# Kernel tuning notes

Hardware: AMD Instinct MI355X
Metric: run time of the kernel (lower is better)

Reference implementation:

```python
import jax, jax.numpy as jnp
import numpy as np

B, T, D, K = 4, 4096, 384, 64

def setup_inputs() -> dict:
    key = jax.random.key(0)
    k1, k2, k3, k4 = jax.random.split(key, 4)
    x = jax.random.normal(k1, (B, T, D), dtype=jnp.float32)
    # nn.Linear weights stored as (out_features, in_features); y = x @ W.T
    Wk = jax.random.normal(k2, (K, D), dtype=jnp.float32) * (1.0 / np.sqrt(D))
    Wq = jax.random.normal(k3, (K, D), dtype=jnp.float32) * (1.0 / np.sqrt(D))
    Wv = jax.random.normal(k4, (D, D), dtype=jnp.float32) * (1.0 / np.sqrt(D))
    return {"x": x, "Wk": Wk, "Wq": Wq, "Wv": Wv}

def reference(x, Wk, Wq, Wv):
    # x: (B,T,D)
    k = jnp.einsum('btd,kd->btk', x, Wk)   # (B,T,K)
    q = jnp.einsum('btd,kd->btk', x, Wq)   # (B,T,K)
    v = jnp.einsum('btd,ed->bte', x, Wv)   # (B,T,D)
    scores = jnp.einsum('btk,bsk->bts', q, k)  # (B,T,T)
    Tq = x.shape[1]
    causal = jnp.tril(jnp.ones((Tq, Tq), dtype=bool))[None, :, :]
    scores = jnp.where(causal, scores, -jnp.inf)
    w = jax.nn.softmax(scores / jnp.sqrt(jnp.asarray(Wk.shape[0], scores.dtype)), axis=-1)
    return jnp.einsum('bts,bsd->btd', w, v)  # (B,T,D)
```

## Files before the change

### kernel.cpp

```cpp
#include <hip/hip_runtime.h>


#define BB 4
#define TT 4096
#define DD 384

#define OWKA 0
#define OWQA 24576
#define OWVB 49152
#define OYK  196608
#define OYQ  1245184
#define OVT  2293760

#define C_EXP 0.18033688011112042f

typedef __bf16 bf16x8 __attribute__((ext_vector_type(8)));
typedef float f32x16 __attribute__((ext_vector_type(16)));
typedef unsigned short u16x4 __attribute__((ext_vector_type(4)));

__device__ __forceinline__ unsigned short f2bf(float f) {
  unsigned int u = __builtin_bit_cast(unsigned int, f);
  u += 0x7FFFu + ((u >> 16) & 1u);
  return (unsigned short)(u >> 16);
}

__device__ __forceinline__ bf16x8 ldb8(const unsigned short* p) {
  return *reinterpret_cast<const bf16x8*>(p);
}

__global__ __launch_bounds__(256) void convert_w(
    const float* __restrict__ Wk, const float* __restrict__ Wq,
    const float* __restrict__ Wv, unsigned short* __restrict__ ws) {
  int g = blockIdx.x * 256 + threadIdx.x;
  int row = g / 96;
  int fin = (g - row * 96) * 4;
  const float* src;
  unsigned short* dstbase;
  int m;
  if (row < 64)       { src = Wk + row * 384;         dstbase = ws + OWKA; m = row; }
  else if (row < 128) { src = Wq + (row - 64) * 384;  dstbase = ws + OWQA; m = row - 64; }
  else                { src = Wv + (row - 128) * 384; dstbase = ws + OWVB; m = row - 128; }
  float4 f = *reinterpret_cast<const float4*>(src + fin);
  u16x4 o;
  o[0] = f2bf(f.x); o[1] = f2bf(f.y); o[2] = f2bf(f.z); o[3] = f2bf(f.w);
  unsigned short* dst = dstbase + (m >> 5) * 12288 + (fin >> 4) * 512
                        + ((((fin >> 3) & 1) << 5) + (m & 31)) * 8 + (fin & 7);
  *reinterpret_cast<u16x4*>(dst) = o;
}

__global__ __launch_bounds__(512) void proj_fused(
    const float* __restrict__ x, const unsigned short* __restrict__ ws_r,
    unsigned short* __restrict__ Yk, unsigned short* __restrict__ Yq,
    unsigned short* __restrict__ Vt) {
  __shared__ __align__(16) unsigned short xlds[24576];
  int tb = blockIdx.x;
  int b = tb >> 6;
  int tid = threadIdx.x;
  {
    int r = tid >> 3, e = tid & 7;
    const float* xr = x + (tb * 64 + r) * DD + e * 48;
#pragma unroll
    for (int i = 0; i < 12; i++) {
      int fin = e * 48 + i * 4;
      float4 f = *reinterpret_cast<const float4*>(xr + i * 4);
      u16x4 o;
      o[0] = f2bf(f.x); o[1] = f2bf(f.y); o[2] = f2bf(f.z); o[3] = f2bf(f.w);
      unsigned short* dst = xlds + (r >> 5) * 12288 + (fin >> 4) * 512
                            + ((((fin >> 3) & 1) << 5) + (r & 31)) * 8 + (fin & 7);
      *reinterpret_cast<u16x4*>(dst) = o;
    }
  }
  __syncthreads();
  int wid = tid >> 6, lane = tid & 63;
  int l31 = lane & 31, h8 = lane >> 5;
  const f32x16 fz16 = {};
  if (wid < 2) {
    const unsigned short* Wa = ws_r + (wid ? OWQA : OWKA) + lane * 8;
    unsigned short* Ysel = (wid ? Yq : Yk);
    f32x16 acc[2][2];
    acc[0][0] = fz16; acc[0][1] = fz16; acc[1][0] = fz16; acc[1][1] = fz16;
    for (int ks = 0; ks < 24; ks++) {
      bf16x8 a0 = ldb8(Wa + ks * 512);
      bf16x8 a1 = ldb8(Wa + 12288 + ks * 512);
      bf16x8 b0 = ldb8(xlds + ks * 512 + lane * 8);
      bf16x8 b1 = ldb8(xlds + 12288 + ks * 512 + lane * 8);
      acc[0][0] = __builtin_amdgcn_mfma_f32_32x32x16_bf16(a0, b0, acc[0][0], 0, 0, 0);
      acc[0][1] = __builtin_amdgcn_mfma_f32_32x32x16_bf16(a0, b1, acc[0][1], 0, 0, 0);
      acc[1][0] = __builtin_amdgcn_mfma_f32_32x32x16_bf16(a1, b0, acc[1][0], 0, 0, 0);
      acc[1][1] = __builtin_amdgcn_mfma_f32_32x32x16_bf16(a1, b1, acc[1][1], 0, 0, 0);
    }
#pragma unroll
    for (int mt = 0; mt < 2; mt++)
#pragma unroll
      for (int nt = 0; nt < 2; nt++) {
        int tile = b * 128 + (tb & 63) * 2 + nt;
#pragma unroll
        for (int rg = 0; rg < 4; rg++) {
          u16x4 o;
#pragma unroll
          for (int i = 0; i < 4; i++) o[i] = f2bf(acc[mt][nt][rg * 4 + i]);
          *reinterpret_cast<u16x4*>(Ysel + tile * 2048 + (mt * 2 + (rg >> 1)) * 512
                                    + (((rg & 1) << 5) + l31) * 8 + 4 * h8) = o;
        }
      }
  } else {
    int vw = wid - 2;
    const unsigned short* Wb = ws_r + OWVB + vw * 2 * 12288 + lane * 8;
    f32x16 acc[2][2];
    acc[0][0] = fz16; acc[0][1] = fz16; acc[1][0] = fz16; acc[1][1] = fz16;
    for (int ks = 0; ks < 24; ks++) {
      bf16x8 a0 = ldb8(xlds + ks * 512 + lane * 8);
      bf16x8 a1 = ldb8(xlds + 12288 + ks * 512 + lane * 8);
      bf16x8 w0 = ldb8(Wb + ks * 512);
      bf16x8 w1 = ldb8(Wb + 12288 + ks * 512);
      acc[0][0] = __builtin_amdgcn_mfma_f32_32x32x16_bf16(a0, w0, acc[0][0], 0, 0, 0);
      acc[0][1] = __builtin_amdgcn_mfma_f32_32x32x16_bf16(a0, w1, acc[0][1], 0, 0, 0);
      acc[1][0] = __builtin_amdgcn_mfma_f32_32x32x16_bf16(a1, w0, acc[1][0], 0, 0, 0);
      acc[1][1] = __builtin_amdgcn_mfma_f32_32x32x16_bf16(a1, w1, acc[1][1], 0, 0, 0);
    }
    int k128 = (tb & 63) >> 1;
#pragma unroll
    for (int t32 = 0; t32 < 2; t32++)
#pragma unroll
      for (int dt = 0; dt < 2; dt++) {
        int dti = vw * 2 + dt;
        unsigned short* vbase = Vt + ((b * 12 + dti) * 32 + k128) * 4096;
#pragma unroll
        for (int rg = 0; rg < 4; rg++) {
          u16x4 o;
#pragma unroll
          for (int i = 0; i < 4; i++) o[i] = f2bf(acc[t32][dt][rg * 4 + i]);
          int kseg = 4 * (tb & 1) + t32 * 2 + (rg >> 1);
          *reinterpret_cast<u16x4*>(vbase + kseg * 512
                                    + (((rg & 1) << 5) + l31) * 8 + 4 * h8) = o;
        }
      }
  }
}

__global__ __launch_bounds__(256, 2) void flash_attn(
    const unsigned short* __restrict__ Yk, const unsigned short* __restrict__ Yq,
    const unsigned short* __restrict__ Vt, float* __restrict__ out) {
  __shared__ __align__(16) unsigned short pbuf[2][8192];
  __shared__ float lred[4][32];
  int blk = blockIdx.x;
  int xcd = blk & 7;
  int b = xcd >> 1, half = xcd & 1;
  int n = blk >> 3;
  int st = (n < 32) ? (127 - 2 * n - half) : (2 * (n - 32) + half);
  int wid = threadIdx.x >> 6, lane = threadIdx.x & 63;
  int l31 = lane & 31, h8 = lane >> 5;
  const f32x16 fz16 = {};
  const unsigned short* qbase = Yq + (b * 128 + st) * 2048 + lane * 8;
  bf16x8 qf[4];
#pragma unroll
  for (int ks = 0; ks < 4; ks++) qf[ks] = ldb8(qbase + ks * 512);
  f32x16 acc[3];
  acc[0] = fz16; acc[1] = fz16; acc[2] = fz16;
  float psum = 0.f;
  int n128 = (st >> 2) + 1;
  int qrow = st * 32 + l31;
  const unsigned short* kbase = Yk + (b * 128 + wid) * 2048 + lane * 8;
  const unsigned short* vbase = Vt + ((b * 12 + wid * 3) * 32) * 4096 + lane * 8;
#pragma unroll 1
  for (int kb = 0; kb < n128; kb++) {
    const unsigned short* kt = kbase + kb * 8192;
    bf16x8 kf[4];
#pragma unroll
    for (int ks = 0; ks < 4; ks++) kf[ks] = ldb8(kt + ks * 512);
    f32x16 sacc = fz16;
#pragma unroll
    for (int ks = 0; ks < 4; ks++)
      sacc = __builtin_amdgcn_mfma_f32_32x32x16_bf16(kf[ks], qf[ks], sacc, 0, 0, 0);
    int kg0 = kb * 128 + wid * 32 + 4 * h8;
    unsigned short* pw = pbuf[kb & 1];
#pragma unroll
    for (int rg = 0; rg < 4; rg++) {
      u16x4 o;
#pragma unroll
      for (int i = 0; i < 4; i++) {
        int key = kg0 + rg * 8 + i;
        float pv = (key > qrow) ? 0.f : exp2f(sacc[rg * 4 + i] * C_EXP);
        psum += pv;
        o[i] = f2bf(pv);
      }
      int g = wid * 2 + (rg >> 1);
      *reinterpret_cast<u16x4*>(pw + g * 512 + ((rg & 1) * 32 + l31) * 8 + 4 * h8) = o;
    }
    const unsigned short* vt = vbase + kb * 4096;
    bf16x8 vf0[8], vf1[8], vf2[8];
#pragma unroll
    for (int g = 0; g < 8; g++) vf0[g] = ldb8(vt + g * 512);
#pragma unroll
    for (int g = 0; g < 8; g++) vf1[g] = ldb8(vt + 32 * 4096 + g * 512);
#pragma unroll
    for (int g = 0; g < 8; g++) vf2[g] = ldb8(vt + 64 * 4096 + g * 512);
    __syncthreads();
    bf16x8 pf[8];
#pragma unroll
    for (int g = 0; g < 8; g++) pf[g] = ldb8(pw + g * 512 + lane * 8);
#pragma unroll
    for (int g = 0; g < 8; g++) {
      acc[0] = __builtin_amdgcn_mfma_f32_32x32x16_bf16(vf0[g], pf[g], acc[0], 0, 0, 0);
      acc[1] = __builtin_amdgcn_mfma_f32_32x32x16_bf16(vf1[g], pf[g], acc[1], 0, 0, 0);
      acc[2] = __builtin_amdgcn_mfma_f32_32x32x16_bf16(vf2[g], pf[g], acc[2], 0, 0, 0);
    }
  }
  psum += __shfl_xor(psum, 32);
  if (h8 == 0) lred[wid][l31] = psum;
  __syncthreads();
  float lt = lred[0][l31] + lred[1][l31] + lred[2][l31] + lred[3][l31];
  float inv = 1.0f / lt;
  float* ob = out + (b * TT + st * 32 + l31) * DD + wid * 96;
#pragma unroll
  for (int dt = 0; dt < 3; dt++)
#pragma unroll
    for (int rg = 0; rg < 4; rg++) {
      float4 o4;
      o4.x = acc[dt][rg * 4 + 0] * inv; o4.y = acc[dt][rg * 4 + 1] * inv;
      o4.z = acc[dt][rg * 4 + 2] * inv; o4.w = acc[dt][rg * 4 + 3] * inv;
      *reinterpret_cast<float4*>(ob + dt * 32 + rg * 8 + h8 * 4) = o4;
    }
}

extern "C" void kernel_launch(void* const* d_in, const int* in_sizes, int n_in,
                              void* d_out, int out_size, void* d_ws, size_t ws_size,
                              hipStream_t stream) {
  const float* x  = (const float*)d_in[0];
  const float* Wk = (const float*)d_in[1];
  const float* Wq = (const float*)d_in[2];
  const float* Wv = (const float*)d_in[3];
  unsigned short* ws = (unsigned short*)d_ws;
  unsigned short* Yk = ws + OYK;
  unsigned short* Yq = ws + OYQ;
  unsigned short* Vt = ws + OVT;

  convert_w<<<192, 256, 0, stream>>>(Wk, Wq, Wv, ws);
  proj_fused<<<256, 512, 0, stream>>>(x, ws, Yk, Yq, Vt);
  flash_attn<<<512, 256, 0, stream>>>(Yk, Yq, Vt, (float*)d_out);
}
```

Before: 153.7 us.

## Split key blocks across two wave groups per block with LDS reduction

The flash attention kernel now uses 512 threads per block: two groups of four waves each handle alternating 128-key blocks for the same query tile, then merge their partial PV accumulators through LDS before writing output. Block-to-tile scheduling is also changed from an XCD-aware interleave to a simple heavy-first order by batch. The aim is to halve the serial key loop per block and raise the number of waves resident per CU to hide latency. The cost is extra LDS for per-group P buffers, a three-step synchronized reduction at the end, possible idle waves when the number of key blocks is odd, and the loss of the XCD locality mapping.

```diff
diff --git a/kernel.cpp b/kernel.cpp
--- a/kernel.cpp
+++ b/kernel.cpp
@@ -138,17 +138,18 @@
   }
 }
 
-__global__ __launch_bounds__(256, 2) void flash_attn(
+__global__ __launch_bounds__(512, 4) void flash_attn(
     const unsigned short* __restrict__ Yk, const unsigned short* __restrict__ Yq,
     const unsigned short* __restrict__ Vt, float* __restrict__ out) {
-  __shared__ __align__(16) unsigned short pbuf[2][8192];
-  __shared__ float lred[4][32];
+  __shared__ __align__(16) unsigned short pbuf[2][2][8192];
+  __shared__ float lred[8][32];
   int blk = blockIdx.x;
-  int xcd = blk & 7;
-  int b = xcd >> 1, half = xcd & 1;
-  int n = blk >> 3;
-  int st = (n < 32) ? (127 - 2 * n - half) : (2 * (n - 32) + half);
-  int wid = threadIdx.x >> 6, lane = threadIdx.x & 63;
+  int b = blk & 3;
+  int idx = blk >> 2;
+  int st = (blk < 256) ? (127 - idx) : (idx - 64);
+  int tid = threadIdx.x;
+  int wid = tid >> 6, lane = tid & 63;
+  int dq = wid & 3, kh = wid >> 2;
   int l31 = lane & 31, h8 = lane >> 5;
   const f32x16 fz16 = {};
   const unsigned short* qbase = Yq + (b * 128 + st) * 2048 + lane * 8;
@@ -159,68 +160,100 @@
   acc[0] = fz16; acc[1] = fz16; acc[2] = fz16;
   float psum = 0.f;
   int n128 = (st >> 2) + 1;
+  int nI = (n128 + 1) >> 1;
   int qrow = st * 32 + l31;
-  const unsigned short* kbase = Yk + (b * 128 + wid) * 2048 + lane * 8;
-  const unsigned short* vbase = Vt + ((b * 12 + wid * 3) * 32) * 4096 + lane * 8;
+  const unsigned short* kbase = Yk + (b * 128 + dq) * 2048 + lane * 8;
+  const unsigned short* vbase = Vt + ((b * 12 + dq * 3) * 32) * 4096 + lane * 8;
 #pragma unroll 1
-  for (int kb = 0; kb < n128; kb++) {
-    const unsigned short* kt = kbase + kb * 8192;
-    bf16x8 kf[4];
-#pragma unroll
-    for (int ks = 0; ks < 4; ks++) kf[ks] = ldb8(kt + ks * 512);
-    f32x16 sacc = fz16;
-#pragma unroll
-    for (int ks = 0; ks < 4; ks++)
-      sacc = __builtin_amdgcn_mfma_f32_32x32x16_bf16(kf[ks], qf[ks], sacc, 0, 0, 0);
-    int kg0 = kb * 128 + wid * 32 + 4 * h8;
-    unsigned short* pw = pbuf[kb & 1];
-#pragma unroll
-    for (int rg = 0; rg < 4; rg++) {
-      u16x4 o;
-#pragma unroll
-      for (int i = 0; i < 4; i++) {
-        int key = kg0 + rg * 8 + i;
-        float pv = (key > qrow) ? 0.f : exp2f(sacc[rg * 4 + i] * C_EXP);
-        psum += pv;
-        o[i] = f2bf(pv);
-      }
-      int g = wid * 2 + (rg >> 1);
-      *reinterpret_cast<u16x4*>(pw + g * 512 + ((rg & 1) * 32 + l31) * 8 + 4 * h8) = o;
-    }
-    const unsigned short* vt = vbase + kb * 4096;
+  for (int i = 0; i < nI; i++) {
+    int kb = 2 * i + kh;
+    bool active = kb < n128;
+    unsigned short* pw = pbuf[kh][i & 1];
     bf16x8 vf0[8], vf1[8], vf2[8];
-#pragma unroll
-    for (int g = 0; g < 8; g++) vf0[g] = ldb8(vt + g * 512);
-#pragma unroll
-    for (int g = 0; g < 8; g++) vf1[g] = ldb8(vt + 32 * 4096 + g * 512);
-#pragma unroll
-    for (int g = 0; g < 8; g++) vf2[g] = ldb8(vt + 64 * 4096 + g * 512);
+    if (active) {
+      const unsigned short* kt = kbase + kb * 8192;
+      bf16x8 kf[4];
+#pragma unroll
+      for (int ks = 0; ks < 4; ks++) kf[ks] = ldb8(kt + ks * 512);
+      f32x16 sacc = fz16;
+#pragma unroll
+      for (int ks = 0; ks < 4; ks++)
+        sacc = __builtin_amdgcn_mfma_f32_32x32x16_bf16(kf[ks], qf[ks], sacc, 0, 0, 0);
+      const unsigned short* vt = vbase + kb * 4096;
+#pragma unroll
+      for (int g = 0; g < 8; g++) vf0[g] = ldb8(vt + g * 512);
+#pragma unroll
+      for (int g = 0; g < 8; g++) vf1[g] = ldb8(vt + 32 * 4096 + g * 512);
+#pragma unroll
+      for (int g = 0; g < 8; g++) vf2[g] = ldb8(vt + 64 * 4096 + g * 512);
+      int kg0 = kb * 128 + dq * 32 + 4 * h8;
+#pragma unroll
+      for (int rg = 0; rg < 4; rg++) {
+        u16x4 o;
+#pragma unroll
+        for (int j = 0; j < 4; j++) {
+          int key = kg0 + rg * 8 + j;
+          float pv = (key > qrow) ? 0.f : exp2f(sacc[rg * 4 + j] * C_EXP);
+          psum += pv;
+          o[j] = f2bf(pv);
+        }
+        int g = dq * 2 + (rg >> 1);
+        *reinterpret_cast<u16x4*>(pw + g * 512 + ((rg & 1) * 32 + l31) * 8 + 4 * h8) = o;
+      }
+    }
     __syncthreads();
-    bf16x8 pf[8];
-#pragma unroll
-    for (int g = 0; g < 8; g++) pf[g] = ldb8(pw + g * 512 + lane * 8);
-#pragma unroll
-    for (int g = 0; g < 8; g++) {
-      acc[0] = __builtin_amdgcn_mfma_f32_32x32x16_bf16(vf0[g], pf[g], acc[0], 0, 0, 0);
-      acc[1] = __builtin_amdgcn_mfma_f32_32x32x16_bf16(vf1[g], pf[g], acc[1], 0, 0, 0);
-      acc[2] = __builtin_amdgcn_mfma_f32_32x32x16_bf16(vf2[g], pf[g], acc[2], 0, 0, 0);
+    if (active) {
+#pragma unroll
+      for (int g = 0; g < 8; g++) {
+        bf16x8 pf = ldb8(pw + g * 512 + lane * 8);
+        acc[0] = __builtin_amdgcn_mfma_f32_32x32x16_bf16(vf0[g], pf, acc[0], 0, 0, 0);
+        acc[1] = __builtin_amdgcn_mfma_f32_32x32x16_bf16(vf1[g], pf, acc[1], 0, 0, 0);
+        acc[2] = __builtin_amdgcn_mfma_f32_32x32x16_bf16(vf2[g], pf, acc[2], 0, 0, 0);
+      }
     }
   }
   psum += __shfl_xor(psum, 32);
   if (h8 == 0) lred[wid][l31] = psum;
   __syncthreads();
-  float lt = lred[0][l31] + lred[1][l31] + lred[2][l31] + lred[3][l31];
-  float inv = 1.0f / lt;
-  float* ob = out + (b * TT + st * 32 + l31) * DD + wid * 96;
-#pragma unroll
-  for (int dt = 0; dt < 3; dt++)
-#pragma unroll
-    for (int rg = 0; rg < 4; rg++) {
-      float4 o4;
-      o4.x = acc[dt][rg * 4 + 0] * inv; o4.y = acc[dt][rg * 4 + 1] * inv;
-      o4.z = acc[dt][rg * 4 + 2] * inv; o4.w = acc[dt][rg * 4 + 3] * inv;
-      *reinterpret_cast<float4*>(ob + dt * 32 + rg * 8 + h8 * 4) = o4;
-    }
+  float lt = lred[0][l31] + lred[1][l31] + lred[2][l31] + lred[3][l31]
+           + lred[4][l31] + lred[5][l31] + lred[6][l31] + lred[7][l31];
+  float* mbuf = (float*)&pbuf[0][0][0];
+#pragma unroll 1
+  for (int dt = 0; dt < 3; dt++) {
+    float* mp = mbuf + dq * 1024 + lane * 16;
+    if (kh == 1) {
+#pragma unroll
+      for (int rg = 0; rg < 4; rg++) {
+        float4 o4;
+        o4.x = acc[dt][rg * 4 + 0]; o4.y = acc[dt][rg * 4 + 1];
+        o4.z = acc[dt][rg * 4 + 2]; o4.w = acc[dt][rg * 4 + 3];
+        *reinterpret_cast<float4*>(mp + rg * 4) = o4;
+      }
+    }
+    __syncthreads();
+    if (kh == 0) {
+#pragma unroll
+      for (int rg = 0; rg < 4; rg++) {
+        float4 o4 = *reinterpret_cast<const float4*>(mp + rg * 4);
+        acc[dt][rg * 4 + 0] += o4.x; acc[dt][rg * 4 + 1] += o4.y;
+        acc[dt][rg * 4 + 2] += o4.z; acc[dt][rg * 4 + 3] += o4.w;
+      }
+    }
+    __syncthreads();
+  }
+  if (kh == 0) {
+    float inv = 1.0f / lt;
+    float* ob = out + (b * TT + st * 32 + l31) * DD + dq * 96;
+#pragma unroll
+    for (int dt = 0; dt < 3; dt++)
+#pragma unroll
+      for (int rg = 0; rg < 4; rg++) {
+        float4 o4;
+        o4.x = acc[dt][rg * 4 + 0] * inv; o4.y = acc[dt][rg * 4 + 1] * inv;
+        o4.z = acc[dt][rg * 4 + 2] * inv; o4.w = acc[dt][rg * 4 + 3] * inv;
+        *reinterpret_cast<float4*>(ob + dt * 32 + rg * 8 + h8 * 4) = o4;
+      }
+  }
 }
 
 extern "C" void kernel_launch(void* const* d_in, const int* in_sizes, int n_in,
@@ -237,5 +270,5 @@
 
   convert_w<<<192, 256, 0, stream>>>(Wk, Wq, Wv, ws);
   proj_fused<<<256, 512, 0, stream>>>(x, ws, Yk, Yq, Vt);
-  flash_attn<<<512, 256, 0, stream>>>(Yk, Yq, Vt, (float*)d_out);
-}
+  flash_attn<<<512, 512, 0, stream>>>(Yk, Yq, Vt, (float*)d_out);
+}
```

Measured after the change: 399.4 us. 160% more time.

## Split long causal query tiles across two blocks and merge partial outputs

Applied to the files above, without the earlier changes.

The upper half of query tiles (st >= 64) now have their key range split between two blocks. One block writes unnormalized fp32 partials plus the row sum, the other writes bf16 partials plus its row sum, and a new merge kernel adds them and normalizes. This raises the block count from 512 to 768 and evens out per-block work to cut tail imbalance, at the cost of an extra kernel launch, extra partial-output traffic, and a bf16 rounding step on half of the partial sums. The x-load loop in the projection kernel is also remapped so consecutive threads read consecutive float4s for coalescing.

```diff
diff --git a/kernel.cpp b/kernel.cpp
--- a/kernel.cpp
+++ b/kernel.cpp
@@ -1,7 +1,6 @@
 #include <hip/hip_runtime.h>
 
 
-#define BB 4
 #define TT 4096
 #define DD 384
 
@@ -11,6 +10,9 @@
 #define OYK  196608
 #define OYQ  1245184
 #define OVT  2293760
+#define OOB  8585216
+#define OLF  11730944
+#define OLB  11747328
 
 #define C_EXP 0.18033688011112042f
 
@@ -22,6 +24,11 @@
   unsigned int u = __builtin_bit_cast(unsigned int, f);
   u += 0x7FFFu + ((u >> 16) & 1u);
   return (unsigned short)(u >> 16);
+}
+
+__device__ __forceinline__ float bf2f(unsigned short s) {
+  unsigned int u = ((unsigned int)s) << 16;
+  return __builtin_bit_cast(float, u);
 }
 
 __device__ __forceinline__ bf16x8 ldb8(const unsigned short* p) {
@@ -57,12 +64,13 @@
   int b = tb >> 6;
   int tid = threadIdx.x;
   {
-    int r = tid >> 3, e = tid & 7;
-    const float* xr = x + (tb * 64 + r) * DD + e * 48;
+    const float* xbase = x + tb * 64 * DD;
 #pragma unroll
     for (int i = 0; i < 12; i++) {
-      int fin = e * 48 + i * 4;
-      float4 f = *reinterpret_cast<const float4*>(xr + i * 4);
+      int idx = tid + 512 * i;
+      int r = idx / 96;
+      int fin = (idx - r * 96) * 4;
+      float4 f = *reinterpret_cast<const float4*>(xbase + idx * 4);
       u16x4 o;
       o[0] = f2bf(f.x); o[1] = f2bf(f.y); o[2] = f2bf(f.z); o[3] = f2bf(f.w);
       unsigned short* dst = xlds + (r >> 5) * 12288 + (fin >> 4) * 512
@@ -140,14 +148,27 @@
 
 __global__ __launch_bounds__(256, 2) void flash_attn(
     const unsigned short* __restrict__ Yk, const unsigned short* __restrict__ Yq,
-    const unsigned short* __restrict__ Vt, float* __restrict__ out) {
+    const unsigned short* __restrict__ Vt, float* __restrict__ out,
+    unsigned short* __restrict__ obk, float* __restrict__ lf, float* __restrict__ lb) {
   __shared__ __align__(16) unsigned short pbuf[2][8192];
   __shared__ float lred[4][32];
   int blk = blockIdx.x;
-  int xcd = blk & 7;
-  int b = xcd >> 1, half = xcd & 1;
-  int n = blk >> 3;
-  int st = (n < 32) ? (127 - 2 * n - half) : (2 * (n - 32) + half);
+  int b, st, kb0, kb1, mode, n128;
+  if (blk < 512) {
+    b = blk & 3;
+    int u = blk >> 2;
+    st = 127 - (u >> 1);
+    n128 = (st >> 2) + 1;
+    int front = (n128 + 1) >> 1;
+    if ((u & 1) == 0) { kb0 = 0; kb1 = front; mode = 1; }
+    else              { kb0 = front; kb1 = n128; mode = 2; }
+  } else {
+    int v = blk - 512;
+    b = v & 3;
+    st = 63 - (v >> 2);
+    n128 = (st >> 2) + 1;
+    kb0 = 0; kb1 = n128; mode = 0;
+  }
   int wid = threadIdx.x >> 6, lane = threadIdx.x & 63;
   int l31 = lane & 31, h8 = lane >> 5;
   const f32x16 fz16 = {};
@@ -158,12 +179,11 @@
   f32x16 acc[3];
   acc[0] = fz16; acc[1] = fz16; acc[2] = fz16;
   float psum = 0.f;
-  int n128 = (st >> 2) + 1;
   int qrow = st * 32 + l31;
   const unsigned short* kbase = Yk + (b * 128 + wid) * 2048 + lane * 8;
   const unsigned short* vbase = Vt + ((b * 12 + wid * 3) * 32) * 4096 + lane * 8;
 #pragma unroll 1
-  for (int kb = 0; kb < n128; kb++) {
+  for (int kb = kb0; kb < kb1; kb++) {
     const unsigned short* kt = kbase + kb * 8192;
     bf16x8 kf[4];
 #pragma unroll
@@ -178,11 +198,11 @@
     for (int rg = 0; rg < 4; rg++) {
       u16x4 o;
 #pragma unroll
-      for (int i = 0; i < 4; i++) {
-        int key = kg0 + rg * 8 + i;
-        float pv = (key > qrow) ? 0.f : exp2f(sacc[rg * 4 + i] * C_EXP);
+      for (int j = 0; j < 4; j++) {
+        int key = kg0 + rg * 8 + j;
+        float pv = (key > qrow) ? 0.f : exp2f(sacc[rg * 4 + j] * C_EXP);
         psum += pv;
-        o[i] = f2bf(pv);
+        o[j] = f2bf(pv);
       }
       int g = wid * 2 + (rg >> 1);
       *reinterpret_cast<u16x4*>(pw + g * 512 + ((rg & 1) * 32 + l31) * 8 + 4 * h8) = o;
@@ -210,17 +230,66 @@
   if (h8 == 0) lred[wid][l31] = psum;
   __syncthreads();
   float lt = lred[0][l31] + lred[1][l31] + lred[2][l31] + lred[3][l31];
-  float inv = 1.0f / lt;
-  float* ob = out + (b * TT + st * 32 + l31) * DD + wid * 96;
-#pragma unroll
-  for (int dt = 0; dt < 3; dt++)
-#pragma unroll
-    for (int rg = 0; rg < 4; rg++) {
-      float4 o4;
-      o4.x = acc[dt][rg * 4 + 0] * inv; o4.y = acc[dt][rg * 4 + 1] * inv;
-      o4.z = acc[dt][rg * 4 + 2] * inv; o4.w = acc[dt][rg * 4 + 3] * inv;
-      *reinterpret_cast<float4*>(ob + dt * 32 + rg * 8 + h8 * 4) = o4;
-    }
+  if (mode == 0) {
+    float inv = 1.0f / lt;
+    float* ob = out + (b * TT + st * 32 + l31) * DD + wid * 96;
+#pragma unroll
+    for (int dt = 0; dt < 3; dt++)
+#pragma unroll
+      for (int rg = 0; rg < 4; rg++) {
+        float4 o4;
+        o4.x = acc[dt][rg * 4 + 0] * inv; o4.y = acc[dt][rg * 4 + 1] * inv;
+        o4.z = acc[dt][rg * 4 + 2] * inv; o4.w = acc[dt][rg * 4 + 3] * inv;
+        *reinterpret_cast<float4*>(ob + dt * 32 + rg * 8 + h8 * 4) = o4;
+      }
+  } else if (mode == 1) {
+    float* ob = out + (b * TT + st * 32 + l31) * DD + wid * 96;
+#pragma unroll
+    for (int dt = 0; dt < 3; dt++)
+#pragma unroll
+      for (int rg = 0; rg < 4; rg++) {
+        float4 o4;
+        o4.x = acc[dt][rg * 4 + 0]; o4.y = acc[dt][rg * 4 + 1];
+        o4.z = acc[dt][rg * 4 + 2]; o4.w = acc[dt][rg * 4 + 3];
+        *reinterpret_cast<float4*>(ob + dt * 32 + rg * 8 + h8 * 4) = o4;
+      }
+    if (wid == 0 && h8 == 0) lf[(b * 64 + st - 64) * 32 + l31] = lt;
+  } else {
+    unsigned short* ob = obk + ((b * 64 + st - 64) * 32 + l31) * DD + wid * 96;
+#pragma unroll
+    for (int dt = 0; dt < 3; dt++)
+#pragma unroll
+      for (int rg = 0; rg < 4; rg++) {
+        u16x4 o;
+#pragma unroll
+        for (int i = 0; i < 4; i++) o[i] = f2bf(acc[dt][rg * 4 + i]);
+        *reinterpret_cast<u16x4*>(ob + dt * 32 + rg * 8 + h8 * 4) = o;
+      }
+    if (wid == 0 && h8 == 0) lb[(b * 64 + st - 64) * 32 + l31] = lt;
+  }
+}
+
+__global__ __launch_bounds__(256) void merge_split(
+    float* __restrict__ out, const unsigned short* __restrict__ obk,
+    const float* __restrict__ lf, const float* __restrict__ lb) {
+  int blk = blockIdx.x;
+  int b = blk >> 6, s = blk & 63;
+  int tid = threadIdx.x;
+  int q = tid >> 3, g = tid & 7;
+  int base = (b * 64 + s) * 32 + q;
+  float inv = 1.0f / (lf[base] + lb[base]);
+  float* ro = out + (b * TT + (64 + s) * 32 + q) * DD + g * 48;
+  const unsigned short* po = obk + base * DD + g * 48;
+#pragma unroll
+  for (int i = 0; i < 12; i++) {
+    float4 o4 = *reinterpret_cast<const float4*>(ro + i * 4);
+    u16x4 p = *reinterpret_cast<const u16x4*>(po + i * 4);
+    o4.x = (o4.x + bf2f(p[0])) * inv;
+    o4.y = (o4.y + bf2f(p[1])) * inv;
+    o4.z = (o4.z + bf2f(p[2])) * inv;
+    o4.w = (o4.w + bf2f(p[3])) * inv;
+    *reinterpret_cast<float4*>(ro + i * 4) = o4;
+  }
 }
 
 extern "C" void kernel_launch(void* const* d_in, const int* in_sizes, int n_in,
@@ -231,11 +300,15 @@
   const float* Wq = (const float*)d_in[2];
   const float* Wv = (const float*)d_in[3];
   unsigned short* ws = (unsigned short*)d_ws;
-  unsigned short* Yk = ws + OYK;
-  unsigned short* Yq = ws + OYQ;
-  unsigned short* Vt = ws + OVT;
+  unsigned short* Yk  = ws + OYK;
+  unsigned short* Yq  = ws + OYQ;
+  unsigned short* Vt  = ws + OVT;
+  unsigned short* obk = ws + OOB;
+  float* lf = (float*)(ws + OLF);
+  float* lb = (float*)(ws + OLB);
 
   convert_w<<<192, 256, 0, stream>>>(Wk, Wq, Wv, ws);
   proj_fused<<<256, 512, 0, stream>>>(x, ws, Yk, Yq, Vt);
-  flash_attn<<<512, 256, 0, stream>>>(Yk, Yq, Vt, (float*)d_out);
-}
+  flash_attn<<<768, 256, 0, stream>>>(Yk, Yq, Vt, (float*)d_out, obk, lf, lb);
+  merge_split<<<256, 256, 0, stream>>>((float*)d_out, obk, lf, lb);
+}
```

New measurement: 162.0 us. 1.05x slower.
